# Performance work log

Hardware: AMD Instinct MI355X
Metric: run time of the kernel (lower is better)

## Reference

```python
import jax, jax.numpy as jnp
import numpy as np


def _batch_conv2d(inputs, kernels):
    # inputs: [B, 1, H, W], kernels: [B, 1, 3, 3]; distinct kernel per sample
    # Implemented as a grouped conv: view inputs as [1, B, H, W], groups=B.
    B, _, H, W = inputs.shape
    out = jax.lax.conv_general_dilated(
        inputs.reshape(1, B, H, W),
        kernels,  # OIHW with O=B, I=1
        window_strides=(1, 1),
        padding=((1, 1), (1, 1)),
        feature_group_count=B,
        dimension_numbers=("NCHW", "OIHW", "NCHW"),
    )
    return out.reshape(B, 1, H, W)


def setup_inputs() -> dict:
    key = jax.random.key(0)
    k1, k2, k3 = jax.random.split(key, 3)
    B, m = 64, 512
    x = jax.random.normal(k1, (B, 1, m, m), dtype=jnp.float32)
    f = jax.random.normal(k2, (B, 1, m, m), dtype=jnp.float32)
    kernelA = jax.random.normal(k3, (B, 1, 3, 3), dtype=jnp.float32)
    return {"x": x, "f": f, "kernelA": kernelA}


def reference(x, f, kernelA):
    # One Jacobi-style smoothing step: x <- x + (f - A x) / 6
    Ax = _batch_conv2d(x, kernelA)
    x = x + (f - Ax) * (1.0 / 6.0)
    return x
```

## Files before the change

kernel.cpp:

```cpp
#include <hip/hip_runtime.h>

#define BB 64
#define HH 512
#define WW 512
#define W4 (WW / 4)

struct RowE { float4 v; float l, r; };

__device__ __forceinline__ RowE load_row(const float* __restrict__ xrow,
                                         int j0, int lane) {
    RowE r;
    r.v = *(const float4*)(xrow + j0);
    float lh = __shfl_up(r.v.w, 1);
    float rh = __shfl_down(r.v.x, 1);
    if (lane == 0)  lh = (j0 > 0)      ? xrow[j0 - 1] : 0.f;
    if (lane == 63) rh = (j0 + 4 < WW) ? xrow[j0 + 4] : 0.f;
    r.l = lh; r.r = rh;
    return r;
}

__device__ __forceinline__ RowE zero_row() {
    RowE r;
    r.v = make_float4(0.f, 0.f, 0.f, 0.f);
    r.l = 0.f; r.r = 0.f;
    return r;
}

__global__ __launch_bounds__(256) void jacobi_v4_kernel(
    const float* __restrict__ x,
    const float* __restrict__ f,
    const float* __restrict__ k,
    float* __restrict__ out)
{
    const int tid  = threadIdx.x;
    const int lane = tid & 63;

    const int b = blockIdx.x >> 8;
    const int q = ((blockIdx.x & 255) << 8) + tid;
    const int j4 = q & (W4 - 1);
    const int i  = q >> 7;
    const int j0 = j4 << 2;

    const size_t img = (size_t)b * HH * WW;
    const float* xb = x + img;

    const float* kb = k + b * 9;
    const float k00 = kb[0], k01 = kb[1], k02 = kb[2];
    const float k10 = kb[3], k11 = kb[4], k12 = kb[5];
    const float k20 = kb[6], k21 = kb[7], k22 = kb[8];

    const RowE c = load_row(xb + (size_t)i * WW, j0, lane);
    const RowE m = (i > 0)      ? load_row(xb + (size_t)(i - 1) * WW, j0, lane)
                                : zero_row();
    const RowE p = (i < HH - 1) ? load_row(xb + (size_t)(i + 1) * WW, j0, lane)
                                : zero_row();

    float4 acc;
    acc.x = k00 * m.l   + k01 * m.v.x + k02 * m.v.y
          + k10 * c.l   + k11 * c.v.x + k12 * c.v.y
          + k20 * p.l   + k21 * p.v.x + k22 * p.v.y;
    acc.y = k00 * m.v.x + k01 * m.v.y + k02 * m.v.z
          + k10 * c.v.x + k11 * c.v.y + k12 * c.v.z
          + k20 * p.v.x + k21 * p.v.y + k22 * p.v.z;
    acc.z = k00 * m.v.y + k01 * m.v.z + k02 * m.v.w
          + k10 * c.v.y + k11 * c.v.z + k12 * c.v.w
          + k20 * p.v.y + k21 * p.v.z + k22 * p.v.w;
    acc.w = k00 * m.v.z + k01 * m.v.w + k02 * m.r
          + k10 * c.v.z + k11 * c.v.w + k12 * c.r
          + k20 * p.v.z + k21 * p.v.w + k22 * p.r;

    const size_t idx4 = (size_t)b * HH * W4 + (size_t)i * W4 + j4;
    const float4 fv = ((const float4*)f)[idx4];

    const float inv6 = 1.f / 6.f;
    float4 o;
    o.x = c.v.x + (fv.x - acc.x) * inv6;
    o.y = c.v.y + (fv.y - acc.y) * inv6;
    o.z = c.v.z + (fv.z - acc.z) * inv6;
    o.w = c.v.w + (fv.w - acc.w) * inv6;

    ((float4*)out)[idx4] = o;
}

extern "C" void kernel_launch(void* const* d_in, const int* in_sizes, int n_in,
                              void* d_out, int out_size, void* d_ws, size_t ws_size,
                              hipStream_t stream) {
    const float* x = (const float*)d_in[0];
    const float* f = (const float*)d_in[1];
    const float* kk = (const float*)d_in[2];
    float* out = (float*)d_out;

    const int blocks = (BB * HH * W4) / 256;
    jacobi_v4_kernel<<<blocks, 256, 0, stream>>>(x, f, kk, out);
}
```

Measured before the change: 166.5 us.

## Compute two output rows per thread and swizzle block order across XCDs

Each thread now computes two vertically adjacent output rows, loading four input rows instead of three per row, which cuts redundant row loads of x. Each block covers four rows of one image, and block indices are remapped so that consecutive logical blocks land on the same XCD (nb&7 interleave), keeping neighbouring rows' halo reuse in a shared L2. Work per thread doubles and the grid halves, which raises register use and lowers the number of waves in flight.

```diff
diff --git a/kernel.cpp b/kernel.cpp
--- a/kernel.cpp
+++ b/kernel.cpp
@@ -26,7 +26,29 @@
     return r;
 }
 
-__global__ __launch_bounds__(256) void jacobi_v4_kernel(
+__device__ __forceinline__ float4 stencil(
+    const RowE& t, const RowE& c, const RowE& bo,
+    float k00, float k01, float k02,
+    float k10, float k11, float k12,
+    float k20, float k21, float k22)
+{
+    float4 acc;
+    acc.x = k00 * t.l   + k01 * t.v.x + k02 * t.v.y
+          + k10 * c.l   + k11 * c.v.x + k12 * c.v.y
+          + k20 * bo.l  + k21 * bo.v.x + k22 * bo.v.y;
+    acc.y = k00 * t.v.x + k01 * t.v.y + k02 * t.v.z
+          + k10 * c.v.x + k11 * c.v.y + k12 * c.v.z
+          + k20 * bo.v.x + k21 * bo.v.y + k22 * bo.v.z;
+    acc.z = k00 * t.v.y + k01 * t.v.z + k02 * t.v.w
+          + k10 * c.v.y + k11 * c.v.z + k12 * c.v.w
+          + k20 * bo.v.y + k21 * bo.v.z + k22 * bo.v.w;
+    acc.w = k00 * t.v.z + k01 * t.v.w + k02 * t.r
+          + k10 * c.v.z + k11 * c.v.w + k12 * c.r
+          + k20 * bo.v.z + k21 * bo.v.w + k22 * bo.r;
+    return acc;
+}
+
+__global__ __launch_bounds__(256) void jacobi_v5_kernel(
     const float* __restrict__ x,
     const float* __restrict__ f,
     const float* __restrict__ k,
@@ -35,11 +57,17 @@
     const int tid  = threadIdx.x;
     const int lane = tid & 63;
 
-    const int b = blockIdx.x >> 8;
-    const int q = ((blockIdx.x & 255) << 8) + tid;
-    const int j4 = q & (W4 - 1);
-    const int i  = q >> 7;
-    const int j0 = j4 << 2;
+    const int nb      = blockIdx.x;
+    const int logical = (nb & 7) * 1024 + (nb >> 3);
+
+    const int b   = logical >> 7;
+    const int blk = logical & 127;
+    const int r0  = blk << 2;
+
+    const int half = tid >> 7;
+    const int j4   = tid & 127;
+    const int j0   = j4 << 2;
+    const int r    = r0 + (half << 1);
 
     const size_t img = (size_t)b * HH * WW;
     const float* xb = x + img;
@@ -49,47 +77,43 @@
     const float k10 = kb[3], k11 = kb[4], k12 = kb[5];
     const float k20 = kb[6], k21 = kb[7], k22 = kb[8];
 
-    const RowE c = load_row(xb + (size_t)i * WW, j0, lane);
-    const RowE m = (i > 0)      ? load_row(xb + (size_t)(i - 1) * WW, j0, lane)
-                                : zero_row();
-    const RowE p = (i < HH - 1) ? load_row(xb + (size_t)(i + 1) * WW, j0, lane)
-                                : zero_row();
+    const RowE ra = (r > 0)      ? load_row(xb + (size_t)(r - 1) * WW, j0, lane)
+                                 : zero_row();
+    const RowE rb = load_row(xb + (size_t)r * WW, j0, lane);
+    const RowE rc = load_row(xb + (size_t)(r + 1) * WW, j0, lane);
+    const RowE rd = (r + 2 < HH) ? load_row(xb + (size_t)(r + 2) * WW, j0, lane)
+                                 : zero_row();
 
-    float4 acc;
-    acc.x = k00 * m.l   + k01 * m.v.x + k02 * m.v.y
-          + k10 * c.l   + k11 * c.v.x + k12 * c.v.y
-          + k20 * p.l   + k21 * p.v.x + k22 * p.v.y;
-    acc.y = k00 * m.v.x + k01 * m.v.y + k02 * m.v.z
-          + k10 * c.v.x + k11 * c.v.y + k12 * c.v.z
-          + k20 * p.v.x + k21 * p.v.y + k22 * p.v.z;
-    acc.z = k00 * m.v.y + k01 * m.v.z + k02 * m.v.w
-          + k10 * c.v.y + k11 * c.v.z + k12 * c.v.w
-          + k20 * p.v.y + k21 * p.v.z + k22 * p.v.w;
-    acc.w = k00 * m.v.z + k01 * m.v.w + k02 * m.r
-          + k10 * c.v.z + k11 * c.v.w + k12 * c.r
-          + k20 * p.v.z + k21 * p.v.w + k22 * p.r;
+    const size_t idx0 = (size_t)b * HH * W4 + (size_t)r * W4 + j4;
+    const float4 f0 = ((const float4*)f)[idx0];
+    const float4 f1 = ((const float4*)f)[idx0 + W4];
 
-    const size_t idx4 = (size_t)b * HH * W4 + (size_t)i * W4 + j4;
-    const float4 fv = ((const float4*)f)[idx4];
+    const float4 a0 = stencil(ra, rb, rc, k00,k01,k02, k10,k11,k12, k20,k21,k22);
+    const float4 a1 = stencil(rb, rc, rd, k00,k01,k02, k10,k11,k12, k20,k21,k22);
 
     const float inv6 = 1.f / 6.f;
-    float4 o;
-    o.x = c.v.x + (fv.x - acc.x) * inv6;
-    o.y = c.v.y + (fv.y - acc.y) * inv6;
-    o.z = c.v.z + (fv.z - acc.z) * inv6;
-    o.w = c.v.w + (fv.w - acc.w) * inv6;
+    float4 o0, o1;
+    o0.x = rb.v.x + (f0.x - a0.x) * inv6;
+    o0.y = rb.v.y + (f0.y - a0.y) * inv6;
+    o0.z = rb.v.z + (f0.z - a0.z) * inv6;
+    o0.w = rb.v.w + (f0.w - a0.w) * inv6;
+    o1.x = rc.v.x + (f1.x - a1.x) * inv6;
+    o1.y = rc.v.y + (f1.y - a1.y) * inv6;
+    o1.z = rc.v.z + (f1.z - a1.z) * inv6;
+    o1.w = rc.v.w + (f1.w - a1.w) * inv6;
 
-    ((float4*)out)[idx4] = o;
+    ((float4*)out)[idx0]      = o0;
+    ((float4*)out)[idx0 + W4] = o1;
 }
 
 extern "C" void kernel_launch(void* const* d_in, const int* in_sizes, int n_in,
                               void* d_out, int out_size, void* d_ws, size_t ws_size,
                               hipStream_t stream) {
-    const float* x = (const float*)d_in[0];
-    const float* f = (const float*)d_in[1];
+    const float* x  = (const float*)d_in[0];
+    const float* f  = (const float*)d_in[1];
     const float* kk = (const float*)d_in[2];
     float* out = (float*)d_out;
 
-    const int blocks = (BB * HH * W4) / 256;
-    jacobi_v4_kernel<<<blocks, 256, 0, stream>>>(x, f, kk, out);
+    const int blocks = BB * (HH / 4);
+    jacobi_v5_kernel<<<blocks, 256, 0, stream>>>(x, f, kk, out);
 }
```

New measurement: 174.3 us. 1.05x slower.
